# Performance work log

Hardware: AMD Instinct MI355X
Metric: run time of the kernel (lower is better)

## Reference

```python
import jax, jax.numpy as jnp
import numpy as np

D_MODEL = 1024
N_HEAD = 16
HEAD_DIM = D_MODEL // N_HEAD
D_FF = 4096
N_EXPERTS = 4
EPS = 1e-05


def _layer_norm(x, gamma, beta):
    mu = jnp.mean(x, axis=-1, keepdims=True)
    var = jnp.mean((x - mu) ** 2, axis=-1, keepdims=True)
    return (x - mu) / jnp.sqrt(var + EPS) * gamma + beta


def setup_inputs() -> dict:
    key = jax.random.key(0)
    ks = jax.random.split(key, 20)
    f32 = jnp.float32
    sc = 1.0 / np.sqrt(D_MODEL)
    scf = 1.0 / np.sqrt(D_FF)
    return {
        "src": jax.random.normal(ks[0], (4, 512, D_MODEL), f32),
        "Wq": jax.random.normal(ks[1], (D_MODEL, D_MODEL), f32) * sc,
        "bq": jnp.zeros((D_MODEL,), f32),
        "Wk": jax.random.normal(ks[2], (D_MODEL, D_MODEL), f32) * sc,
        "bk": jnp.zeros((D_MODEL,), f32),
        "Wv": jax.random.normal(ks[3], (D_MODEL, D_MODEL), f32) * sc,
        "bv": jnp.zeros((D_MODEL,), f32),
        "Wo": jax.random.normal(ks[4], (D_MODEL, D_MODEL), f32) * sc,
        "bo": jnp.zeros((D_MODEL,), f32),
        "router_w": jax.random.normal(ks[5], (D_MODEL, 1), f32) * 0.05,
        "router_b": jnp.zeros((1,), f32),
        "W1": jax.random.normal(ks[6], (N_EXPERTS, D_MODEL, D_FF), f32) * sc,
        "b1": jnp.zeros((N_EXPERTS, D_FF), f32),
        "W2": jax.random.normal(ks[7], (N_EXPERTS, D_FF, D_MODEL), f32) * scf,
        "b2": jnp.zeros((N_EXPERTS, D_MODEL), f32),
        "ln1_g": jnp.ones((D_MODEL,), f32),
        "ln1_b": jnp.zeros((D_MODEL,), f32),
        "ln2_g": jnp.ones((D_MODEL,), f32),
        "ln2_b": jnp.zeros((D_MODEL,), f32),
    }


def reference(src, Wq, bq, Wk, bk, Wv, bv, Wo, bo, router_w, router_b,
              W1, b1, W2, b2, ln1_g, ln1_b, ln2_g, ln2_b):
    B, T, _ = src.shape
    # --- self attention ---
    q = (src @ Wq + bq).reshape(B, T, N_HEAD, HEAD_DIM)
    k = (src @ Wk + bk).reshape(B, T, N_HEAD, HEAD_DIM)
    v = (src @ Wv + bv).reshape(B, T, N_HEAD, HEAD_DIM)
    scale = HEAD_DIM ** -0.5
    scores = jnp.einsum('bqhd,bkhd->bhqk', q, k) * scale
    probs = jax.nn.softmax(scores, axis=-1)
    attn = jnp.einsum('bhqk,bkhd->bqhd', probs, v).reshape(B, T, D_MODEL)
    attn = attn @ Wo + bo
    x = _layer_norm(src + attn, ln1_g, ln1_b)
    # --- hash-routed single-expert MoE FFN ---
    keys = (x @ router_w + router_b)[..., 0]           # [B, T]
    expert_idx = jnp.remainder(jnp.floor(keys).astype(jnp.int32), N_EXPERTS)
    ff_out = jnp.zeros_like(x)
    for e in range(N_EXPERTS):
        h = jax.nn.relu(x @ W1[e] + b1[e])             # [B, T, D_FF]
        y = h @ W2[e] + b2[e]                          # [B, T, D_MODEL]
        ff_out = ff_out + jnp.where((expert_idx == e)[..., None], y, 0.0)
    return _layer_norm(x + ff_out, ln2_g, ln2_b)
```

## Files before the change

### kernel.cpp

```cpp
#include <hip/hip_runtime.h>
#include <hip/hip_bf16.h>
#include <stdint.h>

typedef unsigned short u16;
typedef __attribute__((ext_vector_type(8))) short s8v;
typedef __attribute__((ext_vector_type(4))) float f4v;

#define DEVI static __device__ __forceinline__

DEVI u16 f2bf(float x) {
  union { float f; unsigned u; } a; a.f = x;
  return (u16)((a.u + 0x7fffu + ((a.u >> 16) & 1u)) >> 16);
}
DEVI float bf2f(u16 h) {
  union { float f; unsigned u; } a; a.u = ((unsigned)h) << 16; return a.f;
}
DEVI float wred_add(float s) {
#pragma unroll
  for (int o = 32; o; o >>= 1) s += __shfl_xor(s, o, 64);
  return s;
}
DEVI float wred_max(float s) {
#pragma unroll
  for (int o = 32; o; o >>= 1) s = fmaxf(s, __shfl_xor(s, o, 64));
  return s;
}
DEVI f4v mfma16(s8v a, s8v b, f4v c) {
  return __builtin_amdgcn_mfma_f32_16x16x32_bf16(a, b, c, 0, 0, 0);
}

DEVI int rho(int j) { return ((j & 12) << 1) | (j & 3) | ((j >> 4) << 2); }

DEVI void gload16(const u16* gp, u16* lp) {
  __builtin_amdgcn_global_load_lds(
      (const __attribute__((address_space(1))) uint32_t*)gp,
      (__attribute__((address_space(3))) uint32_t*)lp, 16, 0, 0);
}

DEVI s8v ldfrag_sw(const u16* base, int r, int lg) {
  int off = ((r >> 4) << 9) + ((r & 15) << 5) + ((lg ^ ((r >> 1) & 3)) << 3);
  return *(const s8v*)(base + off);
}

template<bool LO>
DEVI void tsplit_body(const float* __restrict__ in, u16* __restrict__ outH, u16* __restrict__ outL,
                      int cc, int rr, int R, int C, float (*t)[132], int id) {
#pragma unroll
  for (int i = 0; i < 4; ++i) {
    int slot = i * 256 + id;
    int r = slot >> 5, c4 = slot & 31;
    float4 v = *(const float4*)&in[(long long)(rr + r) * C + cc + c4 * 4];
    *(float4*)&t[r][c4 * 4] = v;
  }
  __syncthreads();
#pragma unroll
  for (int i = 0; i < 4; ++i) {
    int slot = i * 256 + id;
    int j = slot >> 3, gs = slot & 7;
    int r0 = gs * 4;
    float v0 = t[r0 + 0][j], v1 = t[r0 + 1][j], v2 = t[r0 + 2][j], v3 = t[r0 + 3][j];
    long long o = (long long)(cc + j) * R + rr + 8 * (gs & 3) + 4 * (gs >> 2);
    ushort4 hv;
    hv.x = f2bf(v0); hv.y = f2bf(v1); hv.z = f2bf(v2); hv.w = f2bf(v3);
    *(ushort4*)&outH[o] = hv;
    if (LO) {
      ushort4 lv;
      lv.x = f2bf(v0 - bf2f(hv.x)); lv.y = f2bf(v1 - bf2f(hv.y));
      lv.z = f2bf(v2 - bf2f(hv.z)); lv.w = f2bf(v3 - bf2f(hv.w));
      *(ushort4*)&outL[o] = lv;
    }
  }
}

__global__ __launch_bounds__(256) void prep1_k(const float* __restrict__ src,
    const float* __restrict__ Wq, const float* __restrict__ Wk,
    const float* __restrict__ Wv, const float* __restrict__ Wo,
    const float* __restrict__ bq, const float* __restrict__ bk, const float* __restrict__ bv,
    u16* __restrict__ srcH, u16* __restrict__ srcL,
    u16* __restrict__ WqkvTh, u16* __restrict__ WqkvTl,
    u16* __restrict__ WoTh, u16* __restrict__ WoTl, float* __restrict__ bqkv) {
  __shared__ float tbuf[32][132];
  const int bid = blockIdx.x, tid = threadIdx.x;
  if (bid < 2048) {
    int i = bid * 256 + tid;
    float4 v = ((const float4*)src)[i];
    ushort4 hv, lv;
    hv.x = f2bf(v.x); lv.x = f2bf(v.x - bf2f(hv.x));
    hv.y = f2bf(v.y); lv.y = f2bf(v.y - bf2f(hv.y));
    hv.z = f2bf(v.z); lv.z = f2bf(v.z - bf2f(hv.z));
    hv.w = f2bf(v.w); lv.w = f2bf(v.w - bf2f(hv.w));
    int t = i & 7, blk = i >> 3;
    int si = blk * 8 + ((t & 3) << 1) + (t >> 2);
    ((ushort4*)srcH)[si] = hv;
    ((ushort4*)srcL)[si] = lv;
  } else if (bid < 3072) {
    int t = bid - 2048;
    int wsel = t >> 8, tb = t & 255;
    const float* in = wsel == 0 ? Wq : wsel == 1 ? Wk : wsel == 2 ? Wv : Wo;
    u16* oh = wsel < 3 ? WqkvTh + wsel * 1024 * 1024 : WoTh;
    u16* ol = wsel < 3 ? WqkvTl + wsel * 1024 * 1024 : WoTl;
    tsplit_body<true>(in, oh, ol, (tb & 7) * 128, (tb >> 3) * 32, 1024, 1024, tbuf, tid);
  } else {
    int i = (bid - 3072) * 256 + tid;
    bqkv[i] = i < 1024 ? bq[i] : (i < 2048 ? bk[i - 1024] : bv[i - 2048]);
  }
}

__global__ __launch_bounds__(256) void prep2_k(const float* __restrict__ W1, const float* __restrict__ W2,
                                               u16* __restrict__ W1T, u16* __restrict__ W2T) {
  __shared__ float tbuf[32][132];
  const int bid = blockIdx.x, tid = threadIdx.x;
  if (bid < 4096) {
    int bx = bid & 31, by = (bid >> 5) & 31, bz = bid >> 10;
    tsplit_body<false>(W1 + (long long)bz * 1024 * 4096, W1T + (long long)bz * 4096 * 1024, nullptr,
                       bx * 128, by * 32, 1024, 4096, tbuf, tid);
  } else {
    int t = bid - 4096;
    int bx = t & 7, by = (t >> 3) & 127, bz = t >> 10;
    tsplit_body<false>(W2 + (long long)bz * 4096 * 1024, W2T + (long long)bz * 1024 * 4096, nullptr,
                       bx * 128, by * 32, 4096, 1024, tbuf, tid);
  }
}

__global__ __launch_bounds__(256) void transpose_pair_k(const u16* __restrict__ inH, const u16* __restrict__ inL,
                                                        u16* __restrict__ oH, u16* __restrict__ oL) {
  __shared__ u16 th[32][40], tl[32][40];
  const int b = blockIdx.z;
  const int dd = blockIdx.x * 32;
  const int tt = blockIdx.y * 32;
  const int id = threadIdx.y * 32 + threadIdx.x;
  const int rr = id >> 3, g = id & 7;
  const int rg = 8 * (g & 3) + 4 * (g >> 2);
  const int64_t ibase = ((int64_t)(b * 512 + tt)) * 3072 + 2048 + dd;
  ushort4 hv = *(const ushort4*)&inH[ibase + (int64_t)rr * 3072 + rg];
  ushort4 lv = *(const ushort4*)&inL[ibase + (int64_t)rr * 3072 + rg];
  *(ushort4*)&th[rr][4 * g] = hv;
  *(ushort4*)&tl[rr][4 * g] = lv;
  __syncthreads();
  const int j = rr;
  ushort4 ho, lo;
  ho.x = th[4 * g + 0][j]; ho.y = th[4 * g + 1][j]; ho.z = th[4 * g + 2][j]; ho.w = th[4 * g + 3][j];
  lo.x = tl[4 * g + 0][j]; lo.y = tl[4 * g + 1][j]; lo.z = tl[4 * g + 2][j]; lo.w = tl[4 * g + 3][j];
  const int64_t obase = ((int64_t)b * 1024 + dd + j) * 512 + tt + rg;
  *(ushort4*)&oH[obase] = ho;
  *(ushort4*)&oL[obase] = lo;
}

struct GemmArgs {
  const u16* Ah; const u16* Al; int lda;
  const u16* Bh; const u16* Bl; int ldb;
  float* C; u16* Ch; u16* Cl; int ldc;
  const float* bias;
  int K;
  int Z2;
  int64_t aZ1, aZ2, bZ1, bZ2, cZ1, cZ2;
  const int* ofs;
  int64_t bStrE; int biasStrE;
  int NX, NY, YG;
};

template<int BM, int BN, bool SPLIT, int EPI, bool PN, int MINW, bool SWZ>
__global__ __launch_bounds__(256, MINW) void gemm_k(GemmArgs g) {
  constexpr int ASZ = BM * 32, BSZ = BN * 32;
  constexpr int AN = SPLIT ? 2 * ASZ : ASZ;
  constexpr int BNT = SPLIT ? 2 * BSZ : BSZ;
  constexpr int nA = BM / 16, nB = BN / 16;
  constexpr int nAt = SPLIT ? 2 * nA : nA;
  constexpr int TOT = nAt + (SPLIT ? 2 * nB : nB);
  static_assert(TOT % 4 == 0, "chunk count must divide across 4 waves");
  constexpr int NLOAD = TOT / 4;
  __shared__ __align__(16) u16 sA[2][AN];
  __shared__ __align__(16) u16 sB[2][BNT];

  const int tid = threadIdx.x;
  int bx, by, bz;
  if (SWZ) {
    const int nwg = gridDim.x;
    int wg = (blockIdx.x & 7) * (nwg >> 3) + (blockIdx.x >> 3);
    int byl = wg % g.YG; int t = wg / g.YG;
    bx = t % g.NX; t /= g.NX;
    const int nyg = g.NY / g.YG;
    by = (t % nyg) * g.YG + byl;
    bz = t / nyg;
  } else {
    bx = blockIdx.x; by = blockIdx.y; bz = blockIdx.z;
  }

  const u16* Ah = g.Ah; const u16* Al = g.Al;
  const u16* Bh = g.Bh; const u16* Bl = g.Bl;
  int64_t cOff = 0;
  if (g.Z2 > 0) {
    int z1 = bz / g.Z2, z2 = bz % g.Z2;
    int64_t ao = (int64_t)z1 * g.aZ1 + (int64_t)z2 * g.aZ2;
    int64_t bo = (int64_t)z1 * g.bZ1 + (int64_t)z2 * g.bZ2;
    Ah += ao; Bh += bo;
    if (SPLIT) { Al += ao; Bl += bo; }
    cOff = (int64_t)z1 * g.cZ1 + (int64_t)z2 * g.cZ2;
  }
  const int row0 = bx * BM;
  const int col0 = by * BN;
  const float* bias = g.bias;
  if (g.ofs) {
    if (row0 >= g.ofs[4]) return;
    int e = 0;
    while (e < 3 && row0 >= g.ofs[e + 1]) ++e;
    Bh += (int64_t)e * g.bStrE;
    if (bias) bias += (int64_t)e * g.biasStrE;
  }

  const int w = tid >> 6, lane = tid & 63;
  const int wr = w >> 1, wc = w & 1;
  const int lr = lane & 15, lg = lane >> 4;
  constexpr int FM = BM / 32, FN = BN / 32;

  const int srow = lane >> 2;
  const int sG = (lane & 3) ^ ((lane >> 3) & 3);

  auto stage = [&](int b, int kt) {
#pragma unroll
    for (int c = 0; c < NLOAD; ++c) {
      int s = c * 4 + w;
      if (s < nA) {
        int64_t go = (int64_t)(row0 + s * 16 + srow) * g.lda + kt + sG * 8;
        gload16(Ah + go, &sA[b][s * 512]);
      } else if (SPLIT && s < 2 * nA) {
        int ch = s - nA;
        int64_t go = (int64_t)(row0 + ch * 16 + srow) * g.lda + kt + sG * 8;
        gload16(Al + go, &sA[b][ASZ + ch * 512]);
      } else if (s < nAt + nB) {
        int ch = s - nAt;
        int64_t go = (int64_t)(col0 + ch * 16 + srow) * g.ldb + kt + sG * 8;
        gload16(Bh + go, &sB[b][ch * 512]);
      } else {
        int ch = s - nAt - nB;
        int64_t go = (int64_t)(col0 + ch * 16 + srow) * g.ldb + kt + sG * 8;
        gload16(Bl + go, &sB[b][BSZ + ch * 512]);
      }
    }
  };

  f4v acc[FM][FN];
#pragma unroll
  for (int i = 0; i < FM; ++i)
#pragma unroll
    for (int j = 0; j < FN; ++j) acc[i][j] = f4v{0.f, 0.f, 0.f, 0.f};

  s8v a0[FM], b0[FN], al0[SPLIT ? FM : 1], bl0[SPLIT ? FN : 1];
  s8v a1[FM], b1[FN], al1[SPLIT ? FM : 1], bl1[SPLIT ? FN : 1];

  auto rdfrags = [&](int buf, auto& af, auto& bf, auto& afl, auto& bfl) {
#pragma unroll
    for (int mi = 0; mi < FM; ++mi) {
      int r = wr * (BM / 2) + mi * 16 + lr;
      af[mi] = ldfrag_sw(&sA[buf][0], r, lg);
      if (SPLIT) afl[mi] = ldfrag_sw(&sA[buf][ASZ], r, lg);
    }
#pragma unroll
    for (int ni = 0; ni < FN; ++ni) {
      int r = wc * (BN / 2) + ni * 16 + lr;
      bf[ni] = ldfrag_sw(&sB[buf][0], r, lg);
      if (SPLIT) bfl[ni] = ldfrag_sw(&sB[buf][BSZ], r, lg);
    }
  };

  const int nt = g.K >> 5;

  stage(0, 0);
  stage(1, 32);
  asm volatile("s_waitcnt vmcnt(%0)" :: "n"(NLOAD) : "memory");
  __builtin_amdgcn_sched_barrier(0);
  __builtin_amdgcn_s_barrier();
  rdfrags(0, a0, b0, al0, bl0);

  auto body = [&](int t, auto& cA, auto& cB, auto& cAl, auto& cBl,
                  auto& nA_, auto& nB_, auto& nAl_, auto& nBl_) {
    asm volatile("s_waitcnt lgkmcnt(0)" ::: "memory");
    __builtin_amdgcn_sched_barrier(0);
    __builtin_amdgcn_s_barrier();
    if (t + 2 < nt) stage(t & 1, (t + 2) << 5);
    if (t + 1 < nt) {
      if (t + 2 < nt)
        asm volatile("s_waitcnt vmcnt(%0)" :: "n"(NLOAD) : "memory");
      else
        asm volatile("s_waitcnt vmcnt(0)" ::: "memory");
      __builtin_amdgcn_sched_barrier(0);
      __builtin_amdgcn_s_barrier();
      rdfrags((t + 1) & 1, nA_, nB_, nAl_, nBl_);
    }
    __builtin_amdgcn_sched_barrier(0);
    __builtin_amdgcn_s_setprio(1);
#pragma unroll
    for (int mi = 0; mi < FM; ++mi)
#pragma unroll
      for (int ni = 0; ni < FN; ++ni) {
        acc[mi][ni] = mfma16(cA[mi], cB[ni], acc[mi][ni]);
        if (SPLIT) {
          acc[mi][ni] = mfma16(cA[mi], cBl[ni], acc[mi][ni]);
          acc[mi][ni] = mfma16(cAl[mi], cB[ni], acc[mi][ni]);
        }
      }
    __builtin_amdgcn_s_setprio(0);
  };

  for (int t = 0; t < nt; t += 2) {
    body(t,     a0, b0, al0, bl0, a1, b1, al1, bl1);
    body(t + 1, a1, b1, al1, bl1, a0, b0, al0, bl0);
  }

#pragma unroll
  for (int mi = 0; mi < FM; ++mi) {
    int rbase = row0 + wr * (BM / 2) + mi * 16 + lg * 4;
#pragma unroll
    for (int ni = 0; ni < FN; ++ni) {
      int c = col0 + wc * (BN / 2) + ni * 16 + lr;
      int cs = PN ? ((c & ~31) | rho(c & 31)) : c;
      float bv = bias ? bias[c] : 0.f;
#pragma unroll
      for (int j = 0; j < 4; ++j) {
        int r = rbase + j;
        float v = acc[mi][ni][j] + bv;
        if (EPI == 0) {
          g.C[cOff + (int64_t)r * g.ldc + cs] = v;
        } else if (EPI == 1) {
          u16 h = f2bf(v);
          int64_t o = cOff + (int64_t)r * g.ldc + cs;
          g.Ch[o] = h;
          g.Cl[o] = f2bf(v - bf2f(h));
        } else {
          v = v > 0.f ? v : 0.f;
          g.Ch[cOff + (int64_t)r * g.ldc + cs] = f2bf(v);
        }
      }
    }
  }
}

__global__ __launch_bounds__(256) void softmax_k(float* __restrict__ scores) {
  __shared__ float sm[2][2];
  const int sub = threadIdx.x >> 7;
  const int64_t row = (int64_t)blockIdx.x * 2 + sub;
  float* p = scores + row * 512;
  const int t7 = threadIdx.x & 127, w = t7 >> 6, lane = threadIdx.x & 63;
  float4 v = ((const float4*)p)[t7];
  v.x *= 0.125f; v.y *= 0.125f; v.z *= 0.125f; v.w *= 0.125f;
  float m = wred_max(fmaxf(fmaxf(v.x, v.y), fmaxf(v.z, v.w)));
  if (lane == 0) sm[sub][w] = m;
  __syncthreads();
  m = fmaxf(sm[sub][0], sm[sub][1]);
  float e0 = expf(v.x - m), e1 = expf(v.y - m), e2 = expf(v.z - m), e3 = expf(v.w - m);
  float s = wred_add(e0 + e1 + e2 + e3);
  __syncthreads();
  if (lane == 0) sm[sub][w] = s;
  __syncthreads();
  float inv = 1.f / (sm[sub][0] + sm[sub][1]);
  e0 *= inv; e1 *= inv; e2 *= inv; e3 *= inv;
  u16* ph = (u16*)p;
  ushort4 hv, lv;
  hv.x = f2bf(e0); lv.x = f2bf(e0 - bf2f(hv.x));
  hv.y = f2bf(e1); lv.y = f2bf(e1 - bf2f(hv.y));
  hv.z = f2bf(e2); lv.z = f2bf(e2 - bf2f(hv.z));
  hv.w = f2bf(e3); lv.w = f2bf(e3 - bf2f(hv.w));
  ((ushort4*)ph)[t7] = hv;
  ((ushort4*)(ph + 512))[t7] = lv;
}

__global__ __launch_bounds__(256) void ln_router_k(const float* __restrict__ a, const float* __restrict__ b,
                                                   const float* __restrict__ gm, const float* __restrict__ bt,
                                                   const float* __restrict__ rw, const float* __restrict__ rb,
                                                   float* __restrict__ out, int* __restrict__ eidx) {
  __shared__ float sm[4];
  const int r = blockIdx.x, tid = threadIdx.x;
  const int w = tid >> 6, lane = tid & 63;
  float4 va = ((const float4*)(a + (int64_t)r * 1024))[tid];
  float4 vb = ((const float4*)(b + (int64_t)r * 1024))[tid];
  float x0 = va.x + vb.x, x1 = va.y + vb.y, x2 = va.z + vb.z, x3 = va.w + vb.w;
  float s = wred_add(x0 + x1 + x2 + x3);
  if (lane == 0) sm[w] = s;
  __syncthreads();
  float mu = (sm[0] + sm[1] + sm[2] + sm[3]) * (1.f / 1024.f);
  float d0 = x0 - mu, d1 = x1 - mu, d2 = x2 - mu, d3 = x3 - mu;
  float q = wred_add(d0 * d0 + d1 * d1 + d2 * d2 + d3 * d3);
  __syncthreads();
  if (lane == 0) sm[w] = q;
  __syncthreads();
  float var = (sm[0] + sm[1] + sm[2] + sm[3]) * (1.f / 1024.f);
  float rs = 1.f / sqrtf(var + 1e-5f);
  float4 g4 = ((const float4*)gm)[tid];
  float4 b4 = ((const float4*)bt)[tid];
  float4 o;
  o.x = d0 * rs * g4.x + b4.x;
  o.y = d1 * rs * g4.y + b4.y;
  o.z = d2 * rs * g4.z + b4.z;
  o.w = d3 * rs * g4.w + b4.w;
  ((float4*)(out + (int64_t)r * 1024))[tid] = o;
  float4 w4 = ((const float4*)rw)[tid];
  float p = o.x * w4.x + o.y * w4.y + o.z * w4.z + o.w * w4.w;
  p = wred_add(p);
  __syncthreads();
  if (lane == 0) sm[w] = p;
  __syncthreads();
  if (tid == 0) {
    float key = (sm[0] + sm[1] + sm[2] + sm[3]) + rb[0];
    eidx[r] = (int)floorf(key) & 3;
  }
}

__global__ __launch_bounds__(256) void reduce_ln_k(const float* __restrict__ part, const int* __restrict__ rowsrc,
                                                   const int* __restrict__ ofs, const float* __restrict__ b2,
                                                   const float* __restrict__ xb, const float* __restrict__ gm,
                                                   const float* __restrict__ bt, float* __restrict__ out) {
  __shared__ float sm[4];
  const int r = blockIdx.x;
  if (r >= ofs[4]) return;
  const int s = rowsrc[r];
  if (s < 0) return;
  int e = 0;
  while (e < 3 && r >= ofs[e + 1]) ++e;
  const int tid = threadIdx.x, w = tid >> 6, lane = tid & 63;
  const int64_t RN = 2560ll * 1024;
  float4 v0 = ((const float4*)(part + 0 * RN + (int64_t)r * 1024))[tid];
  float4 v1 = ((const float4*)(part + 1 * RN + (int64_t)r * 1024))[tid];
  float4 bb = ((const float4*)(b2 + (int64_t)e * 1024))[tid];
  float4 va = ((const float4*)(xb + (int64_t)s * 1024))[tid];
  float y0 = (v0.x + v1.x) + bb.x, y1 = (v0.y + v1.y) + bb.y;
  float y2 = (v0.z + v1.z) + bb.z, y3 = (v0.w + v1.w) + bb.w;
  float x0 = va.x + y0, x1 = va.y + y1, x2 = va.z + y2, x3 = va.w + y3;
  float sum = wred_add(x0 + x1 + x2 + x3);
  if (lane == 0) sm[w] = sum;
  __syncthreads();
  float mu = (sm[0] + sm[1] + sm[2] + sm[3]) * (1.f / 1024.f);
  float d0 = x0 - mu, d1 = x1 - mu, d2 = x2 - mu, d3 = x3 - mu;
  float q = wred_add(d0 * d0 + d1 * d1 + d2 * d2 + d3 * d3);
  __syncthreads();
  if (lane == 0) sm[w] = q;
  __syncthreads();
  float var = (sm[0] + sm[1] + sm[2] + sm[3]) * (1.f / 1024.f);
  float rs = 1.f / sqrtf(var + 1e-5f);
  float4 g4 = ((const float4*)gm)[tid];
  float4 b4 = ((const float4*)bt)[tid];
  float4 o;
  o.x = d0 * rs * g4.x + b4.x;
  o.y = d1 * rs * g4.y + b4.y;
  o.z = d2 * rs * g4.z + b4.z;
  o.w = d3 * rs * g4.w + b4.w;
  ((float4*)(out + (int64_t)s * 1024))[tid] = o;
}

__global__ __launch_bounds__(256) void compact_k(const int* __restrict__ eidx,
                                                 int* __restrict__ rowsrc, int* __restrict__ ofs) {
  __shared__ unsigned long long sc[256];
  __shared__ int soff[5];
  const int tid = threadIdx.x;
  int myE[8];
  unsigned long long c = 0;
#pragma unroll
  for (int i = 0; i < 8; ++i) {
    int e = eidx[tid * 8 + i];
    myE[i] = e;
    c += 1ull << (e * 16);
  }
  sc[tid] = c;
  __syncthreads();
  for (int o = 1; o < 256; o <<= 1) {
    unsigned long long v = (tid >= o) ? sc[tid - o] : 0ull;
    __syncthreads();
    sc[tid] += v;
    __syncthreads();
  }
  unsigned long long incl = sc[tid], tot = sc[255];
  unsigned long long excl = incl - c;
  if (tid == 0) {
    int off = 0;
    for (int e = 0; e < 4; ++e) {
      soff[e] = off;
      int cnt = (int)((tot >> (e * 16)) & 0xffff);
      off += (cnt + 127) & ~127;
    }
    soff[4] = off;
    for (int e = 0; e < 5; ++e) ofs[e] = soff[e];
  }
  __syncthreads();
  for (int r = tid; r < 2560; r += 256) rowsrc[r] = -1;
  __threadfence_block();
  __syncthreads();
  int rank[4];
#pragma unroll
  for (int e = 0; e < 4; ++e) rank[e] = (int)((excl >> (e * 16)) & 0xffff);
#pragma unroll
  for (int i = 0; i < 8; ++i) {
    int e = myE[i];
    rowsrc[soff[e] + rank[e]] = tid * 8 + i;
    rank[e]++;
  }
}

__global__ __launch_bounds__(256) void gather_k(const float* __restrict__ x, const int* __restrict__ rowsrc,
                                                const int* __restrict__ ofs, u16* __restrict__ xg) {
  int r = blockIdx.x;
  if (r >= ofs[4]) return;
  int s = rowsrc[r];
  int c = threadIdx.x;
  float4 v = (s >= 0) ? ((const float4*)(x + (int64_t)s * 1024))[c] : float4{0.f, 0.f, 0.f, 0.f};
  ushort4 o;
  o.x = f2bf(v.x); o.y = f2bf(v.y); o.z = f2bf(v.z); o.w = f2bf(v.w);
  int t = c & 7, blk = c >> 3;
  int si = blk * 8 + ((t & 3) << 1) + (t >> 2);
  ((ushort4*)(xg + (int64_t)r * 1024))[si] = o;
}

extern "C" void kernel_launch(void* const* d_in, const int* in_sizes, int n_in,
                              void* d_out, int out_size, void* d_ws, size_t ws_size,
                              hipStream_t stream) {
  const float* src = (const float*)d_in[0];
  const float* Wq  = (const float*)d_in[1];
  const float* bq  = (const float*)d_in[2];
  const float* Wk  = (const float*)d_in[3];
  const float* bk  = (const float*)d_in[4];
  const float* Wv  = (const float*)d_in[5];
  const float* bv  = (const float*)d_in[6];
  const float* Wo  = (const float*)d_in[7];
  const float* bo  = (const float*)d_in[8];
  const float* rw  = (const float*)d_in[9];
  const float* rb  = (const float*)d_in[10];
  const float* W1  = (const float*)d_in[11];
  const float* b1  = (const float*)d_in[12];
  const float* W2  = (const float*)d_in[13];
  const float* b2  = (const float*)d_in[14];
  const float* g1  = (const float*)d_in[15];
  const float* be1 = (const float*)d_in[16];
  const float* g2  = (const float*)d_in[17];
  const float* be2 = (const float*)d_in[18];
  float* out = (float*)d_out;

  char* base = (char*)d_ws;
  size_t off = 0;
  auto alloc = [&](size_t bytes) -> char* {
    char* p = base + off;
    off += (bytes + 255) & ~(size_t)255;
    return p;
  };
  const size_t MB = 1ull << 20;
  u16* srcH = (u16*)alloc(4 * MB);
  u16* srcL = (u16*)alloc(4 * MB);
  u16* WqkvTh = (u16*)alloc(6 * MB);
  u16* WqkvTl = (u16*)alloc(6 * MB);
  u16* WoTh = (u16*)alloc(2 * MB);
  u16* WoTl = (u16*)alloc(2 * MB);
  float* bqkv = (float*)alloc(16 * 1024);
  u16* qkvH = (u16*)alloc(12 * MB);
  u16* qkvL = (u16*)alloc(12 * MB);
  u16* hbuf = (u16*)qkvH;
  u16* vTH = (u16*)alloc(4 * MB); u16* vTL = (u16*)alloc(4 * MB);
  float* scores = (float*)alloc(64 * MB);
  u16* W1T = (u16*)scores;
  u16* W2T = (u16*)scores + 16ull * 1024 * 1024;
  u16* attnH = (u16*)alloc(4 * MB); u16* attnL = (u16*)alloc(4 * MB);
  u16* xg = (u16*)attnH;
  float* woOut = (float*)alloc(8 * MB);
  float* xbuf = (float*)alloc(8 * MB);
  float* partials = (float*)alloc(20 * MB);
  int* eidx   = (int*)alloc(2048 * 4);
  int* rowsrc = (int*)alloc(2560 * 4);
  int* ofs    = (int*)alloc(32);
  (void)ws_size; (void)in_sizes; (void)n_in; (void)out_size;

  dim3 tb(32, 8);

  prep1_k<<<3084, 256, 0, stream>>>(src, Wq, Wk, Wv, Wo, bq, bk, bv,
                                    srcH, srcL, WqkvTh, WqkvTl, WoTh, WoTl, bqkv);

  {
    GemmArgs g{};
    g.Ah = srcH; g.Al = srcL; g.lda = 1024;
    g.Bh = WqkvTh; g.Bl = WqkvTl; g.ldb = 1024;
    g.Ch = qkvH; g.Cl = qkvL; g.ldc = 3072;
    g.bias = bqkv; g.K = 1024; g.Z2 = 0;
    g.NX = 16; g.NY = 32; g.YG = 8;
    gemm_k<128, 96, true, 1, true, 2, true><<<dim3(512), 256, 0, stream>>>(g);
  }
  transpose_pair_k<<<dim3(32, 16, 4), tb, 0, stream>>>(qkvH, qkvL, vTH, vTL);

  {
    GemmArgs g{};
    g.Ah = qkvH; g.Al = qkvL; g.lda = 3072;
    g.Bh = qkvH + 1024; g.Bl = qkvL + 1024; g.ldb = 3072;
    g.C = scores; g.ldc = 512;
    g.K = 64; g.Z2 = 16;
    g.aZ1 = 512ll * 3072; g.aZ2 = 64;
    g.bZ1 = 512ll * 3072; g.bZ2 = 64;
    g.cZ1 = 16ll * 512 * 512; g.cZ2 = 512ll * 512;
    gemm_k<128, 64, true, 0, true, 3, false><<<dim3(4, 8, 64), 256, 0, stream>>>(g);
  }
  softmax_k<<<16384, 256, 0, stream>>>(scores);
  {
    GemmArgs g{};
    g.Ah = (const u16*)scores; g.Al = (const u16*)scores + 512; g.lda = 1024;
    g.Bh = vTH; g.Bl = vTL; g.ldb = 512;
    g.Ch = attnH; g.Cl = attnL; g.ldc = 1024;
    g.K = 512; g.Z2 = 16;
    g.aZ1 = 16ll * 512 * 1024; g.aZ2 = 512ll * 1024;
    g.bZ1 = 1024ll * 512;      g.bZ2 = 64ll * 512;
    g.cZ1 = 512ll * 1024;      g.cZ2 = 64;
    gemm_k<64, 64, true, 1, true, 3, false><<<dim3(8, 1, 64), 256, 0, stream>>>(g);
  }
  {
    GemmArgs g{};
    g.Ah = attnH; g.Al = attnL; g.lda = 1024;
    g.Bh = WoTh; g.Bl = WoTl; g.ldb = 1024;
    g.C = woOut; g.ldc = 1024;
    g.bias = bo; g.K = 1024; g.Z2 = 0;
    gemm_k<64, 64, true, 0, false, 3, false><<<dim3(32, 16, 1), 256, 0, stream>>>(g);
  }
  ln_router_k<<<2048, 256, 0, stream>>>(src, woOut, g1, be1, rw, rb, xbuf, eidx);

  compact_k<<<1, 256, 0, stream>>>(eidx, rowsrc, ofs);
  gather_k<<<2560, 256, 0, stream>>>(xbuf, rowsrc, ofs, xg);

  prep2_k<<<8192, 256, 0, stream>>>(W1, W2, W1T, W2T);

  {
    GemmArgs g{};
    g.Ah = xg; g.lda = 1024;
    g.Bh = W1T; g.ldb = 1024;
    g.Ch = hbuf; g.ldc = 4096;
    g.bias = b1; g.biasStrE = 4096;
    g.K = 1024; g.Z2 = 0;
    g.ofs = ofs; g.bStrE = 4096ll * 1024;
    g.NX = 20; g.NY = 32; g.YG = 16;
    gemm_k<128, 128, false, 2, true, 3, true><<<dim3(640), 256, 0, stream>>>(g);
  }
  {
    GemmArgs g{};
    g.Ah = hbuf; g.lda = 4096;
    g.Bh = W2T; g.ldb = 4096;
    g.C = partials; g.ldc = 1024;
    g.bias = nullptr;
    g.K = 2048; g.Z2 = 2;
    g.aZ1 = 0; g.aZ2 = 2048;
    g.bZ1 = 0; g.bZ2 = 2048;
    g.cZ1 = 0; g.cZ2 = 2560ll * 1024;
    g.ofs = ofs; g.bStrE = 4096ll * 1024;
    g.NX = 20; g.NY = 16; g.YG = 16;
    gemm_k<128, 64, false, 0, false, 3, true><<<dim3(640), 256, 0, stream>>>(g);
  }
  reduce_ln_k<<<2560, 256, 0, stream>>>(partials, rowsrc, ofs, b2, xbuf, g2, be2, out);
}
```

Before: 286.8 us.

## Fuse QK^T scores with softmax and retile W2 GEMM into four-way split-K

```diff
diff --git a/kernel.cpp b/kernel.cpp
--- a/kernel.cpp
+++ b/kernel.cpp
@@ -18,11 +18,6 @@
 DEVI float wred_add(float s) {
 #pragma unroll
   for (int o = 32; o; o >>= 1) s += __shfl_xor(s, o, 64);
-  return s;
-}
-DEVI float wred_max(float s) {
-#pragma unroll
-  for (int o = 32; o; o >>= 1) s = fmaxf(s, __shfl_xor(s, o, 64));
   return s;
 }
 DEVI f4v mfma16(s8v a, s8v b, f4v c) {
@@ -146,6 +141,144 @@
   *(ushort4*)&oL[obase] = lo;
 }
 
+__global__ __launch_bounds__(512, 2) void attn_sm_k(const u16* __restrict__ qkvH,
+                                                    const u16* __restrict__ qkvL,
+                                                    u16* __restrict__ probs) {
+  __shared__ __align__(16) u16 sK[2][16384];
+  __shared__ __align__(16) float smax[128][4];
+  __shared__ __align__(16) float ssum[128][4];
+  const int tid = threadIdx.x;
+  const int w = tid >> 6, lane = tid & 63;
+  const int wq = w >> 2, wt = w & 3;
+  const int lr = lane & 15, lg = lane >> 4;
+  const int bx = blockIdx.x, bh = blockIdx.y;
+  const int64_t tokBase = (int64_t)(bh >> 4) * 512;
+  const int h = bh & 15;
+  const int qcol = h * 64, kcol = 1024 + h * 64;
+  const int srow = lane >> 2;
+  const int sG = (lane & 3) ^ ((lane >> 3) & 3);
+
+#pragma unroll
+  for (int c = 0; c < 8; ++c) {
+    int s = c * 8 + w;
+    int ks = s >> 5, rb = s & 31;
+    int64_t go = (tokBase + rb * 16 + srow) * 3072 + kcol + ks * 32 + sG * 8;
+    gload16(qkvH + go, &sK[ks][rb * 512]);
+  }
+  __syncthreads();
+
+  f4v acc[4][8];
+#pragma unroll
+  for (int mi = 0; mi < 4; ++mi)
+#pragma unroll
+    for (int ni = 0; ni < 8; ++ni) acc[mi][ni] = f4v{0.f, 0.f, 0.f, 0.f};
+
+#pragma unroll
+  for (int ks = 0; ks < 2; ++ks) {
+    s8v ah[4], al[4];
+#pragma unroll
+    for (int mi = 0; mi < 4; ++mi) {
+      int64_t tok = tokBase + bx * 128 + wq * 64 + mi * 16 + lr;
+      const u16* p = qkvH + tok * 3072 + qcol + ks * 32 + lg * 8;
+      ah[mi] = *(const s8v*)p;
+      al[mi] = *(const s8v*)(qkvL + (p - qkvH));
+    }
+#pragma unroll
+    for (int ni = 0; ni < 8; ++ni) {
+      int r = wt * 128 + ni * 16 + lr;
+      s8v bh_ = ldfrag_sw(&sK[ks][0], r, lg);
+      s8v bl_ = *(const s8v*)(qkvL + (tokBase + r) * 3072 + kcol + ks * 32 + lg * 8);
+#pragma unroll
+      for (int mi = 0; mi < 4; ++mi) {
+        acc[mi][ni] = mfma16(ah[mi], bh_, acc[mi][ni]);
+        acc[mi][ni] = mfma16(ah[mi], bl_, acc[mi][ni]);
+        acc[mi][ni] = mfma16(al[mi], bh_, acc[mi][ni]);
+      }
+    }
+  }
+
+#pragma unroll
+  for (int mi = 0; mi < 4; ++mi)
+#pragma unroll
+    for (int ni = 0; ni < 8; ++ni) {
+      acc[mi][ni][0] *= 0.125f; acc[mi][ni][1] *= 0.125f;
+      acc[mi][ni][2] *= 0.125f; acc[mi][ni][3] *= 0.125f;
+    }
+
+  float rm[4][4];
+#pragma unroll
+  for (int mi = 0; mi < 4; ++mi)
+#pragma unroll
+    for (int j = 0; j < 4; ++j) {
+      float m = acc[mi][0][j];
+#pragma unroll
+      for (int ni = 1; ni < 8; ++ni) m = fmaxf(m, acc[mi][ni][j]);
+#pragma unroll
+      for (int o = 1; o < 16; o <<= 1) m = fmaxf(m, __shfl_xor(m, o, 64));
+      rm[mi][j] = m;
+    }
+  if (lr == 0) {
+#pragma unroll
+    for (int mi = 0; mi < 4; ++mi)
+#pragma unroll
+      for (int j = 0; j < 4; ++j)
+        smax[wq * 64 + mi * 16 + lg * 4 + j][wt] = rm[mi][j];
+  }
+  __syncthreads();
+  float mrow[4][4];
+#pragma unroll
+  for (int mi = 0; mi < 4; ++mi)
+#pragma unroll
+    for (int j = 0; j < 4; ++j) {
+      float4 t4 = *(const float4*)&smax[wq * 64 + mi * 16 + lg * 4 + j][0];
+      mrow[mi][j] = fmaxf(fmaxf(t4.x, t4.y), fmaxf(t4.z, t4.w));
+    }
+
+  float rs_[4][4];
+#pragma unroll
+  for (int mi = 0; mi < 4; ++mi)
+#pragma unroll
+    for (int j = 0; j < 4; ++j) {
+      float s = 0.f;
+#pragma unroll
+      for (int ni = 0; ni < 8; ++ni) {
+        float e = expf(acc[mi][ni][j] - mrow[mi][j]);
+        acc[mi][ni][j] = e;
+        s += e;
+      }
+#pragma unroll
+      for (int o = 1; o < 16; o <<= 1) s += __shfl_xor(s, o, 64);
+      rs_[mi][j] = s;
+    }
+  if (lr == 0) {
+#pragma unroll
+    for (int mi = 0; mi < 4; ++mi)
+#pragma unroll
+      for (int j = 0; j < 4; ++j)
+        ssum[wq * 64 + mi * 16 + lg * 4 + j][wt] = rs_[mi][j];
+  }
+  __syncthreads();
+
+#pragma unroll
+  for (int mi = 0; mi < 4; ++mi)
+#pragma unroll
+    for (int j = 0; j < 4; ++j) {
+      int row = wq * 64 + mi * 16 + lg * 4 + j;
+      float4 t4 = *(const float4*)&ssum[row][0];
+      float inv = 1.f / (((t4.x + t4.y) + t4.z) + t4.w);
+      u16* rp = probs + ((int64_t)bh * 512 + bx * 128 + row) * 1024;
+#pragma unroll
+      for (int ni = 0; ni < 8; ++ni) {
+        int tcol = wt * 128 + ni * 16 + lr;
+        int cs = (tcol & ~31) | rho(tcol & 31);
+        float p = acc[mi][ni][j] * inv;
+        u16 hv = f2bf(p);
+        rp[cs] = hv;
+        rp[512 + cs] = f2bf(p - bf2f(hv));
+      }
+    }
+}
+
 struct GemmArgs {
   const u16* Ah; const u16* Al; int lda;
   const u16* Bh; const u16* Bl; int ldb;
@@ -335,35 +468,6 @@
   }
 }
 
-__global__ __launch_bounds__(256) void softmax_k(float* __restrict__ scores) {
-  __shared__ float sm[2][2];
-  const int sub = threadIdx.x >> 7;
-  const int64_t row = (int64_t)blockIdx.x * 2 + sub;
-  float* p = scores + row * 512;
-  const int t7 = threadIdx.x & 127, w = t7 >> 6, lane = threadIdx.x & 63;
-  float4 v = ((const float4*)p)[t7];
-  v.x *= 0.125f; v.y *= 0.125f; v.z *= 0.125f; v.w *= 0.125f;
-  float m = wred_max(fmaxf(fmaxf(v.x, v.y), fmaxf(v.z, v.w)));
-  if (lane == 0) sm[sub][w] = m;
-  __syncthreads();
-  m = fmaxf(sm[sub][0], sm[sub][1]);
-  float e0 = expf(v.x - m), e1 = expf(v.y - m), e2 = expf(v.z - m), e3 = expf(v.w - m);
-  float s = wred_add(e0 + e1 + e2 + e3);
-  __syncthreads();
-  if (lane == 0) sm[sub][w] = s;
-  __syncthreads();
-  float inv = 1.f / (sm[sub][0] + sm[sub][1]);
-  e0 *= inv; e1 *= inv; e2 *= inv; e3 *= inv;
-  u16* ph = (u16*)p;
-  ushort4 hv, lv;
-  hv.x = f2bf(e0); lv.x = f2bf(e0 - bf2f(hv.x));
-  hv.y = f2bf(e1); lv.y = f2bf(e1 - bf2f(hv.y));
-  hv.z = f2bf(e2); lv.z = f2bf(e2 - bf2f(hv.z));
-  hv.w = f2bf(e3); lv.w = f2bf(e3 - bf2f(hv.w));
-  ((ushort4*)ph)[t7] = hv;
-  ((ushort4*)(ph + 512))[t7] = lv;
-}
-
 __global__ __launch_bounds__(256) void ln_router_k(const float* __restrict__ a, const float* __restrict__ b,
                                                    const float* __restrict__ gm, const float* __restrict__ bt,
                                                    const float* __restrict__ rw, const float* __restrict__ rb,
@@ -420,10 +524,14 @@
   const int64_t RN = 2560ll * 1024;
   float4 v0 = ((const float4*)(part + 0 * RN + (int64_t)r * 1024))[tid];
   float4 v1 = ((const float4*)(part + 1 * RN + (int64_t)r * 1024))[tid];
+  float4 v2 = ((const float4*)(part + 2 * RN + (int64_t)r * 1024))[tid];
+  float4 v3 = ((const float4*)(part + 3 * RN + (int64_t)r * 1024))[tid];
   float4 bb = ((const float4*)(b2 + (int64_t)e * 1024))[tid];
   float4 va = ((const float4*)(xb + (int64_t)s * 1024))[tid];
-  float y0 = (v0.x + v1.x) + bb.x, y1 = (v0.y + v1.y) + bb.y;
-  float y2 = (v0.z + v1.z) + bb.z, y3 = (v0.w + v1.w) + bb.w;
+  float y0 = ((v0.x + v1.x) + v2.x) + v3.x + bb.x;
+  float y1 = ((v0.y + v1.y) + v2.y) + v3.y + bb.y;
+  float y2 = ((v0.z + v1.z) + v2.z) + v3.z + bb.z;
+  float y3 = ((v0.w + v1.w) + v2.w) + v3.w + bb.w;
   float x0 = va.x + y0, x1 = va.y + y1, x2 = va.z + y2, x3 = va.w + y3;
   float sum = wred_add(x0 + x1 + x2 + x3);
   if (lane == 0) sm[w] = sum;
@@ -558,7 +666,7 @@
   u16* xg = (u16*)attnH;
   float* woOut = (float*)alloc(8 * MB);
   float* xbuf = (float*)alloc(8 * MB);
-  float* partials = (float*)alloc(20 * MB);
+  float* partials = (float*)alloc(40 * MB);
   int* eidx   = (int*)alloc(2048 * 4);
   int* rowsrc = (int*)alloc(2560 * 4);
   int* ofs    = (int*)alloc(32);
@@ -580,18 +688,8 @@
   }
   transpose_pair_k<<<dim3(32, 16, 4), tb, 0, stream>>>(qkvH, qkvL, vTH, vTL);
 
-  {
-    GemmArgs g{};
-    g.Ah = qkvH; g.Al = qkvL; g.lda = 3072;
-    g.Bh = qkvH + 1024; g.Bl = qkvL + 1024; g.ldb = 3072;
-    g.C = scores; g.ldc = 512;
-    g.K = 64; g.Z2 = 16;
-    g.aZ1 = 512ll * 3072; g.aZ2 = 64;
-    g.bZ1 = 512ll * 3072; g.bZ2 = 64;
-    g.cZ1 = 16ll * 512 * 512; g.cZ2 = 512ll * 512;
-    gemm_k<128, 64, true, 0, true, 3, false><<<dim3(4, 8, 64), 256, 0, stream>>>(g);
-  }
-  softmax_k<<<16384, 256, 0, stream>>>(scores);
+  attn_sm_k<<<dim3(4, 64), 512, 0, stream>>>(qkvH, qkvL, (u16*)scores);
+
   {
     GemmArgs g{};
     g.Ah = (const u16*)scores; g.Al = (const u16*)scores + 512; g.lda = 1024;
@@ -635,13 +733,13 @@
     g.Bh = W2T; g.ldb = 4096;
     g.C = partials; g.ldc = 1024;
     g.bias = nullptr;
-    g.K = 2048; g.Z2 = 2;
-    g.aZ1 = 0; g.aZ2 = 2048;
-    g.bZ1 = 0; g.bZ2 = 2048;
+    g.K = 1024; g.Z2 = 4;
+    g.aZ1 = 0; g.aZ2 = 1024;
+    g.bZ1 = 0; g.bZ2 = 1024;
     g.cZ1 = 0; g.cZ2 = 2560ll * 1024;
     g.ofs = ofs; g.bStrE = 4096ll * 1024;
-    g.NX = 20; g.NY = 16; g.YG = 16;
-    gemm_k<128, 64, false, 0, false, 3, true><<<dim3(640), 256, 0, stream>>>(g);
+    g.NX = 20; g.NY = 8; g.YG = 8;
+    gemm_k<128, 128, false, 0, false, 3, true><<<dim3(640), 256, 0, stream>>>(g);
   }
   reduce_ln_k<<<2560, 256, 0, stream>>>(partials, rowsrc, ofs, b2, xbuf, g2, be2, out);
 }
```

New measurement: 277.2 us. 1.03x faster.
